# Performance work log

Hardware: AMD Instinct MI355X
Metric: run time of the kernel (lower is better)

Reference implementation:

```python
import jax, jax.numpy as jnp
import numpy as np
from jax.scipy.special import logsumexp

N, M, D = 4096, 4096, 512
MASS = 0.9
REG = 0.1
REG_KL = 0.01
ITERS = 100


def setup_inputs() -> dict:
    key = jax.random.key(0)
    k0, k1 = jax.random.split(key)
    return {
        "ft0": jax.random.normal(k0, (N, D), dtype=jnp.float32),
        "ft1": jax.random.normal(k1, (M, D), dtype=jnp.float32),
        "bin_score": jnp.float32(0.4),
    }


def reference(ft0, ft1, bin_score):
    # all rows have norm >> 1e-8 for randn inputs -> foreground masks are all True
    f0 = ft0 / jnp.linalg.norm(ft0, axis=-1, keepdims=True)
    f1 = ft1 / jnp.linalg.norm(ft1, axis=-1, keepdims=True)
    cos_sim = f0 @ f1.T                       # [N, M]
    n, m = cos_sim.shape

    # partial OT marginals with dustbin mass (get_partial_distributions)
    a = jnp.concatenate([jnp.full((n,), MASS / n, jnp.float32),
                         jnp.array([1.0 - MASS], jnp.float32)])
    b = jnp.concatenate([jnp.full((m,), MASS / m, jnp.float32),
                         jnp.array([1.0 - MASS], jnp.float32)])
    log_mu, log_nu = jnp.log(a), jnp.log(b)   # [n+1], [m+1]

    # augment score matrix with dustbin row/col (get_partial_ot_problem)
    top = jnp.concatenate([cos_sim, jnp.broadcast_to(bin_score, (n, 1))], axis=1)
    bot = jnp.broadcast_to(bin_score, (1, m + 1))
    couplings = jnp.concatenate([top, bot], axis=0)   # [n+1, m+1]

    lmba = 1.0 / REG                         # = 10.0
    phi = REG_KL / (REG_KL + 1.0 / lmba)     # = 0.01 / 0.11
    Z = lmba * couplings

    def body(carry, _):
        u, v = carry
        u = (log_mu - logsumexp(Z + v[None, :] * lmba, axis=1)) / lmba * phi
        v = (log_nu - logsumexp(Z + u[:, None] * lmba, axis=0)) / lmba * phi
        return (u, v), None

    u0 = jnp.zeros((n + 1,), jnp.float32)
    v0 = jnp.zeros((m + 1,), jnp.float32)
    (u, v), _ = jax.lax.scan(body, (u0, v0), None, length=ITERS)

    prob = jnp.exp(Z + u[:, None] * lmba + v[None, :] * lmba)
    # prob_add_bkg with all-True masks: identity placement, zero the corner
    return prob.at[-1, -1].set(0.0)
```

## Files before the change

kernel.cpp:

```cpp
#include <hip/hip_runtime.h>
#include <math.h>

#define Nn 4096
#define Mm 4096
#define Dd 512
#define NP 4097
#define NPB 4104

#define PHI 0.09090909090909091f
#define LMU_IN  (-8.4231266823771690f)
#define LMU_BIN (-2.3025850929940457f)
#define LOG_NP  8.3180489582454150f

typedef __attribute__((ext_vector_type(8))) __bf16 bf16x8;
typedef __attribute__((ext_vector_type(4))) float  f32x4;

__device__ __forceinline__ void load_lds16(const __bf16* g, __bf16* l) {
    __builtin_amdgcn_global_load_lds(
        (__attribute__((address_space(1))) void*)g,
        (__attribute__((address_space(3))) void*)l,
        16, 0, 0);
}

__device__ __forceinline__ float block_allreduce_256(float v, float* sb) {
    #pragma unroll
    for (int off = 32; off > 0; off >>= 1) v += __shfl_down(v, off, 64);
    __syncthreads();
    if ((threadIdx.x & 63) == 0) sb[threadIdx.x >> 6] = v;
    __syncthreads();
    return sb[0] + sb[1] + sb[2] + sb[3];
}

__global__ __launch_bounds__(256) void normalize_bins_kernel(
    const float* __restrict__ F0, const float* __restrict__ F1,
    const float* __restrict__ binp,
    __bf16* __restrict__ A, __bf16* __restrict__ B, _Float16* __restrict__ Ef,
    float* __restrict__ S0, float* __restrict__ TcA) {
    __shared__ float sb[4];
    const int row = blockIdx.x;
    const float* src = (row < Nn) ? (F0 + (size_t)row * Dd)
                                  : (F1 + (size_t)(row - Nn) * Dd);
    __bf16* dst = (row < Nn) ? (A + (size_t)row * Dd)
                             : (B + (size_t)(row - Nn) * Dd);
    const float2 x = ((const float2*)src)[threadIdx.x];
    const float s = block_allreduce_256(x.x * x.x + x.y * x.y, sb);
    const float rn = rsqrtf(s);
    dst[2 * threadIdx.x]     = (__bf16)(x.x * rn);
    dst[2 * threadIdx.x + 1] = (__bf16)(x.y * rn);

    if (row < 17) {
        const int j = row * 256 + threadIdx.x;
        if (j < NP) Ef[(size_t)Nn * NPB + j] = (_Float16)__expf(10.0f * binp[0]);
    } else if (row < 33) {
        const int i = (row - 17) * 256 + threadIdx.x;
        Ef[(size_t)i * NPB + Mm] = (_Float16)__expf(10.0f * binp[0]);
    } else if (row < 50) {
        const int k = (row - 33) * 256 + threadIdx.x;
        if (k < NP) S0[k] = 0.f;
    } else if (row < 67) {
        const int k = (row - 50) * 256 + threadIdx.x;
        if (k < NP) TcA[k] = 0.f;
    }
}

__global__ __launch_bounds__(256) void gemm_rowsum_kernel(
    const __bf16* __restrict__ A, const __bf16* __restrict__ B,
    _Float16* __restrict__ Ef, float* __restrict__ S0) {
    __shared__ __align__(16) __bf16 As[128 * 32];
    __shared__ __align__(16) __bf16 Bs[128 * 32];
    const int tid = threadIdx.x;
    const int l = tid & 63, wv = tid >> 6;
    const int wm = wv >> 1, wn = wv & 1;
    const int ln = l & 15, lq = l >> 4;
    const int row0 = blockIdx.y << 7, col0 = blockIdx.x << 7;

    f32x4 acc[4][4];
    #pragma unroll
    for (int i = 0; i < 4; ++i)
        #pragma unroll
        for (int j = 0; j < 4; ++j) acc[i][j] = (f32x4){0.f, 0.f, 0.f, 0.f};

    const int ch0 = tid, ch1 = 256 + tid;
    const __bf16* a0 = A + (size_t)(row0 + (ch0 >> 2)) * Dd + ((ch0 & 3) << 3);
    const __bf16* a1 = A + (size_t)(row0 + (ch1 >> 2)) * Dd + ((ch1 & 3) << 3);
    const __bf16* b0 = B + (size_t)(col0 + (ch0 >> 2)) * Dd + ((ch0 & 3) << 3);
    const __bf16* b1 = B + (size_t)(col0 + (ch1 >> 2)) * Dd + ((ch1 & 3) << 3);
    __bf16* lA0 = &As[ch0 * 8]; __bf16* lA1 = &As[ch1 * 8];
    __bf16* lB0 = &Bs[ch0 * 8]; __bf16* lB1 = &Bs[ch1 * 8];

    for (int k0 = 0; k0 < Dd; k0 += 32) {
        __syncthreads();
        load_lds16(a0 + k0, lA0);
        load_lds16(a1 + k0, lA1);
        load_lds16(b0 + k0, lB0);
        load_lds16(b1 + k0, lB1);
        __syncthreads();
        bf16x8 af[4], bfr[4];
        #pragma unroll
        for (int mi = 0; mi < 4; ++mi)
            af[mi] = *(const bf16x8*)&As[(wm * 64 + mi * 16 + ln) * 32 + lq * 8];
        #pragma unroll
        for (int ni = 0; ni < 4; ++ni)
            bfr[ni] = *(const bf16x8*)&Bs[(wn * 64 + ni * 16 + ln) * 32 + lq * 8];
        #pragma unroll
        for (int mi = 0; mi < 4; ++mi)
            #pragma unroll
            for (int ni = 0; ni < 4; ++ni)
                acc[mi][ni] = __builtin_amdgcn_mfma_f32_16x16x32_bf16(
                    af[mi], bfr[ni], acc[mi][ni], 0, 0, 0);
    }

    #pragma unroll
    for (int mi = 0; mi < 4; ++mi) {
        #pragma unroll
        for (int r = 0; r < 4; ++r) {
            const int gi = row0 + wm * 64 + mi * 16 + lq * 4 + r;
            _Float16* bRow = Ef + (size_t)gi * NPB + col0 + wn * 64 + ln;
            float rs = 0.f;
            #pragma unroll
            for (int ni = 0; ni < 4; ++ni) {
                const float e = __expf(10.0f * acc[mi][ni][r]);
                bRow[ni * 16] = (_Float16)e;
                rs += e;
            }
            rs += __shfl_down(rs, 8, 64);
            rs += __shfl_down(rs, 4, 64);
            rs += __shfl_down(rs, 2, 64);
            rs += __shfl_down(rs, 1, 64);
            if (ln == 0) atomicAdd(&S0[gi], rs);
        }
    }
}

__global__ __launch_bounds__(256) void col_pass_kernel(
    const _Float16* __restrict__ Ef, const float* __restrict__ S0,
    const float* __restrict__ eUarr, const float* __restrict__ binp,
    float* __restrict__ Tc, const int mode) {
    __shared__ float evl[32];
    const int tid = threadIdx.x;
    const int t = blockIdx.x;
    const int sI = blockIdx.y;
    const int r0 = sI * 32;

    if (tid < 32) {
        const int r = r0 + tid;
        float ev;
        if (mode == 0) {
            const float ebin = __expf(10.0f * binp[0]);
            ev = __expf(PHI * (LMU_IN - __logf(S0[r] + ebin)));
        } else {
            ev = eUarr[r];
        }
        evl[tid] = ev;
    }
    __syncthreads();

    const int j0 = t * 512 + tid * 2;
    const unsigned short* base = (const unsigned short*)Ef;
    float s0 = 0.f, s1 = 0.f;
    #pragma unroll
    for (int k = 0; k < 32; ++k) {
        const int r = r0 + k;
        union { unsigned u; _Float16 h[2]; } e;
        e.u = *(const unsigned*)(base + (size_t)r * NPB + j0);
        const float ev = evl[k];
        s0 += (float)e.h[0] * ev;
        s1 += (float)e.h[1] * ev;
    }

    float ev4096 = 0.f;
    if (sI == 127) {
        ev4096 = (mode == 0)
               ? __expf(PHI * (LMU_BIN - (LOG_NP + 10.0f * binp[0])))
               : eUarr[Nn];
        union { unsigned u; _Float16 h[2]; } e;
        e.u = *(const unsigned*)(base + (size_t)Nn * NPB + j0);
        s0 += (float)e.h[0] * ev4096;
        s1 += (float)e.h[1] * ev4096;
    }
    atomicAdd(&Tc[j0], s0);
    atomicAdd(&Tc[j0 + 1], s1);

    if (t == 0 && tid < 64) {
        float sc = 0.f;
        if (tid < 32)
            sc = (float)Ef[(size_t)(r0 + tid) * NPB + Mm] * evl[tid];
        else if (tid == 32 && sI == 127)
            sc = (float)Ef[(size_t)Nn * NPB + Mm] * ev4096;
        #pragma unroll
        for (int off = 32; off > 0; off >>= 1) sc += __shfl_down(sc, off, 64);
        if (tid == 0) atomicAdd(&Tc[Mm], sc);
    }
}

__global__ __launch_bounds__(256) void row_pass2_kernel(
    const _Float16* __restrict__ Ef, const float* __restrict__ TcA,
    float* __restrict__ eU, float* __restrict__ TcB) {
    __shared__ float sb[4];
    __shared__ float wl[NP];
    const int tid = threadIdx.x;

    for (int j = tid; j < NP; j += 256) {
        const float lnu = (j < Mm) ? LMU_IN : LMU_BIN;
        wl[j] = __expf(PHI * (lnu - __logf(TcA[j])));
    }
    __syncthreads();

    const int i0 = blockIdx.x * 8;
    #pragma unroll 1
    for (int k = 0; k < 8; ++k) {
        const int i = i0 + k;
        if (i >= NP) break;
        const uint4* rowp = (const uint4*)(Ef + (size_t)i * NPB);
        float s = 0.f;
        #pragma unroll
        for (int c = 0; c < 2; ++c) {
            const int chunk = c * 256 + tid;
            union { uint4 u; _Float16 h[8]; } e;
            e.u = rowp[chunk];
            const float4 w0 = *(const float4*)&wl[chunk * 8];
            const float4 w1 = *(const float4*)&wl[chunk * 8 + 4];
            s += (float)e.h[0] * w0.x + (float)e.h[1] * w0.y
               + (float)e.h[2] * w0.z + (float)e.h[3] * w0.w
               + (float)e.h[4] * w1.x + (float)e.h[5] * w1.y
               + (float)e.h[6] * w1.z + (float)e.h[7] * w1.w;
        }
        if (tid == 0) s += (float)Ef[(size_t)i * NPB + Mm] * wl[Mm];
        s = block_allreduce_256(s, sb);
        if (tid == 0) {
            const float lmu = (i < Nn) ? LMU_IN : LMU_BIN;
            eU[i] = __expf(PHI * (lmu - __logf(s)));
        }
    }
    if (tid < 8 && i0 + tid < NP) TcB[i0 + tid] = 0.f;
}

__global__ __launch_bounds__(256) void finish_kernel(
    const _Float16* __restrict__ Ef, const float* __restrict__ eU,
    const float* __restrict__ TcB, float* __restrict__ out) {
    __shared__ float wl[NP];
    const int tid = threadIdx.x;
    for (int j = tid; j < NP; j += 256) {
        const float lnu = (j < Mm) ? LMU_IN : LMU_BIN;
        wl[j] = __expf(PHI * (lnu - __logf(TcB[j])));
    }
    __syncthreads();

    const int i0 = blockIdx.x * 8;
    #pragma unroll 1
    for (int k = 0; k < 8; ++k) {
        const int i = i0 + k;
        if (i >= NP) break;
        const float sU = eU[i];
        const _Float16* erow = Ef + (size_t)i * NPB;
        float* orow = out + (size_t)i * NP;
        for (int j = tid; j < NP; j += 256) {
            float v = (float)erow[j] * sU * wl[j];
            if (i == Nn && j == Mm) v = 0.f;
            orow[j] = v;
        }
    }
}


extern "C" void kernel_launch(void* const* d_in, const int* in_sizes, int n_in,
                              void* d_out, int out_size, void* d_ws, size_t ws_size,
                              hipStream_t stream) {
    const float* ft0 = (const float*)d_in[0];
    const float* ft1 = (const float*)d_in[1];
    const float* bin = (const float*)d_in[2];
    float* out = (float*)d_out;

    const size_t ABF_B = (size_t)Nn * Dd * 2;
    const size_t EBF_B = (size_t)NP * NPB * 2;
    const size_t VEC_B = 16400;
    __bf16*   Abf = (__bf16*)d_ws;
    __bf16*   Bbf = (__bf16*)((char*)d_ws + ABF_B);
    _Float16* Ef  = (_Float16*)((char*)d_ws + 2 * ABF_B);
    float*    eU  = (float*)((char*)d_ws + 2 * ABF_B + EBF_B);
    float*    S0  = (float*)((char*)d_ws + 2 * ABF_B + EBF_B + VEC_B);
    float*    TcA = (float*)((char*)d_ws + 2 * ABF_B + EBF_B + 2 * VEC_B);
    float*    TcB = (float*)((char*)d_ws + 2 * ABF_B + EBF_B + 3 * VEC_B);

    normalize_bins_kernel<<<Nn + Mm, 256, 0, stream>>>(ft0, ft1, bin,
                                                       Abf, Bbf, Ef, S0, TcA);
    gemm_rowsum_kernel<<<dim3(32, 32), 256, 0, stream>>>(Abf, Bbf, Ef, S0);
    col_pass_kernel<<<dim3(8, 128), 256, 0, stream>>>(Ef, S0, eU, bin, TcA, 0);
    row_pass2_kernel<<<513, 256, 0, stream>>>(Ef, TcA, eU, TcB);
    col_pass_kernel<<<dim3(8, 128), 256, 0, stream>>>(Ef, S0, eU, bin, TcB, 1);
    finish_kernel<<<513, 256, 0, stream>>>(Ef, eU, TcB, out);
}
```

Measured before the change: 201.3 us.

## Enlarge GEMM tile to 256x256x64 with double-buffered swizzled LDS

Reworks the cosine-similarity GEMM to use 256x256 output tiles per 512-thread block, with a K step of 64 and double-buffered LDS staging via global_load_lds. An XOR swizzle is applied to LDS column chunks to avoid bank conflicts, and the next tile is prefetched while the current one is computed, leaving one barrier per step. The aim is more data reuse per loaded byte and overlap of loads with MFMA work. The cost is higher register pressure (128 accumulator floats per lane) and only 256 blocks, which is about one wave of work on 256 CUs.

```diff
diff --git a/kernel.cpp b/kernel.cpp
--- a/kernel.cpp
+++ b/kernel.cpp
@@ -63,58 +63,82 @@
     }
 }
 
-__global__ __launch_bounds__(256) void gemm_rowsum_kernel(
+#define BMt 256
+#define BKt 64
+__global__ __launch_bounds__(512) void gemm_rowsum_kernel(
     const __bf16* __restrict__ A, const __bf16* __restrict__ B,
     _Float16* __restrict__ Ef, float* __restrict__ S0) {
-    __shared__ __align__(16) __bf16 As[128 * 32];
-    __shared__ __align__(16) __bf16 Bs[128 * 32];
+    __shared__ __align__(16) __bf16 As[2][BMt * BKt];
+    __shared__ __align__(16) __bf16 Bs[2][BMt * BKt];
     const int tid = threadIdx.x;
     const int l = tid & 63, wv = tid >> 6;
-    const int wm = wv >> 1, wn = wv & 1;
+    const int wm = wv >> 2, wn = wv & 3;
     const int ln = l & 15, lq = l >> 4;
-    const int row0 = blockIdx.y << 7, col0 = blockIdx.x << 7;
-
-    f32x4 acc[4][4];
-    #pragma unroll
-    for (int i = 0; i < 4; ++i)
+    const int row0 = blockIdx.y << 8, col0 = blockIdx.x << 8;
+
+    f32x4 acc[8][4];
+    #pragma unroll
+    for (int i = 0; i < 8; ++i)
         #pragma unroll
         for (int j = 0; j < 4; ++j) acc[i][j] = (f32x4){0.f, 0.f, 0.f, 0.f};
 
-    const int ch0 = tid, ch1 = 256 + tid;
-    const __bf16* a0 = A + (size_t)(row0 + (ch0 >> 2)) * Dd + ((ch0 & 3) << 3);
-    const __bf16* a1 = A + (size_t)(row0 + (ch1 >> 2)) * Dd + ((ch1 & 3) << 3);
-    const __bf16* b0 = B + (size_t)(col0 + (ch0 >> 2)) * Dd + ((ch0 & 3) << 3);
-    const __bf16* b1 = B + (size_t)(col0 + (ch1 >> 2)) * Dd + ((ch1 & 3) << 3);
-    __bf16* lA0 = &As[ch0 * 8]; __bf16* lA1 = &As[ch1 * 8];
-    __bf16* lB0 = &Bs[ch0 * 8]; __bf16* lB1 = &Bs[ch1 * 8];
-
-    for (int k0 = 0; k0 < Dd; k0 += 32) {
+    const __bf16* aSrc[4]; const __bf16* bSrc[4]; int dOff[4];
+    #pragma unroll
+    for (int p = 0; p < 4; ++p) {
+        const int q = tid + p * 512;
+        const int r = q >> 3, c = q & 7;
+        const int cs = c ^ (r & 7);
+        aSrc[p] = A + (size_t)(row0 + r) * Dd + cs * 8;
+        bSrc[p] = B + (size_t)(col0 + r) * Dd + cs * 8;
+        dOff[p] = q * 8;
+    }
+
+    auto STAGE = [&](int buf, int k0) {
+        #pragma unroll
+        for (int p = 0; p < 4; ++p) load_lds16(aSrc[p] + k0, &As[buf][dOff[p]]);
+        #pragma unroll
+        for (int p = 0; p < 4; ++p) load_lds16(bSrc[p] + k0, &Bs[buf][dOff[p]]);
+    };
+
+    auto COMPUTE = [&](int buf) {
+        #pragma unroll
+        for (int ks = 0; ks < 2; ++ks) {
+            bf16x8 bfr[4];
+            #pragma unroll
+            for (int ni = 0; ni < 4; ++ni) {
+                const int r = wn * 64 + ni * 16 + ln;
+                const int pc = (ks * 4 + lq) ^ (ln & 7);
+                bfr[ni] = *(const bf16x8*)&Bs[buf][r * BKt + pc * 8];
+            }
+            #pragma unroll
+            for (int mi = 0; mi < 8; ++mi) {
+                const int r = wm * 128 + mi * 16 + ln;
+                const int pc = (ks * 4 + lq) ^ (ln & 7);
+                const bf16x8 af = *(const bf16x8*)&As[buf][r * BKt + pc * 8];
+                #pragma unroll
+                for (int ni = 0; ni < 4; ++ni)
+                    acc[mi][ni] = __builtin_amdgcn_mfma_f32_16x16x32_bf16(
+                        af, bfr[ni], acc[mi][ni], 0, 0, 0);
+            }
+        }
+    };
+
+    STAGE(0, 0);
+    __syncthreads();
+    int buf = 0;
+    for (int t = 0; t < (Dd / BKt) - 1; ++t) {
+        STAGE(buf ^ 1, (t + 1) * BKt);
+        COMPUTE(buf);
         __syncthreads();
-        load_lds16(a0 + k0, lA0);
-        load_lds16(a1 + k0, lA1);
-        load_lds16(b0 + k0, lB0);
-        load_lds16(b1 + k0, lB1);
-        __syncthreads();
-        bf16x8 af[4], bfr[4];
-        #pragma unroll
-        for (int mi = 0; mi < 4; ++mi)
-            af[mi] = *(const bf16x8*)&As[(wm * 64 + mi * 16 + ln) * 32 + lq * 8];
-        #pragma unroll
-        for (int ni = 0; ni < 4; ++ni)
-            bfr[ni] = *(const bf16x8*)&Bs[(wn * 64 + ni * 16 + ln) * 32 + lq * 8];
-        #pragma unroll
-        for (int mi = 0; mi < 4; ++mi)
-            #pragma unroll
-            for (int ni = 0; ni < 4; ++ni)
-                acc[mi][ni] = __builtin_amdgcn_mfma_f32_16x16x32_bf16(
-                    af[mi], bfr[ni], acc[mi][ni], 0, 0, 0);
-    }
-
-    #pragma unroll
-    for (int mi = 0; mi < 4; ++mi) {
+        buf ^= 1;
+    }
+    COMPUTE(buf);
+
+    #pragma unroll
+    for (int mi = 0; mi < 8; ++mi) {
         #pragma unroll
         for (int r = 0; r < 4; ++r) {
-            const int gi = row0 + wm * 64 + mi * 16 + lq * 4 + r;
+            const int gi = row0 + wm * 128 + mi * 16 + lq * 4 + r;
             _Float16* bRow = Ef + (size_t)gi * NPB + col0 + wn * 64 + ln;
             float rs = 0.f;
             #pragma unroll
@@ -284,7 +308,7 @@
 
     normalize_bins_kernel<<<Nn + Mm, 256, 0, stream>>>(ft0, ft1, bin,
                                                        Abf, Bbf, Ef, S0, TcA);
-    gemm_rowsum_kernel<<<dim3(32, 32), 256, 0, stream>>>(Abf, Bbf, Ef, S0);
+    gemm_rowsum_kernel<<<dim3(16, 16), 512, 0, stream>>>(Abf, Bbf, Ef, S0);
     col_pass_kernel<<<dim3(8, 128), 256, 0, stream>>>(Ef, S0, eU, bin, TcA, 0);
     row_pass2_kernel<<<513, 256, 0, stream>>>(Ef, TcA, eU, TcB);
     col_pass_kernel<<<dim3(8, 128), 256, 0, stream>>>(Ef, S0, eU, bin, TcB, 1);
```

Result: faster. 192.1 us (-4.6%).
